# Kernel tuning notes

Measured on AMD Instinct MI355X. Metric: run time of the kernel, lower is better.

Reference implementation:

```python
import jax, jax.numpy as jnp
import numpy as np

N = 262144      # total nodes
G = 256         # graphs
P = 1024        # nodes per graph (k=None sort pool keeps all)
E = 4194304     # edges
F_IN = 128
H = 32
C = 10          # out capsules / classes
OUT_LEN = 16
IN_LEN = 96     # 3 * 32 concat
NUM_ITERS = 3


def setup_inputs() -> dict:
    key = jax.random.key(0)
    ks = jax.random.split(key, 12)
    x = jax.random.normal(ks[0], (N, F_IN), jnp.float32)
    # edges within each graph of size P
    src = jax.random.randint(ks[1], (E,), 0, N)
    off = jax.random.randint(ks[2], (E,), 0, P)
    dst = (src // P) * P + off
    edge_index = jnp.stack([src, dst]).astype(jnp.int64)
    batch = jnp.repeat(jnp.arange(G), P).astype(jnp.int64)
    W1 = jax.random.normal(ks[3], (F_IN, H), jnp.float32) / np.sqrt(F_IN)
    b1 = jnp.zeros((H,), jnp.float32)
    W2 = jax.random.normal(ks[4], (H, H), jnp.float32) / np.sqrt(H)
    b2 = jnp.zeros((H,), jnp.float32)
    W3 = jax.random.normal(ks[5], (H, H), jnp.float32) / np.sqrt(H)
    b3 = jnp.zeros((H,), jnp.float32)
    caps_W = jax.random.normal(ks[6], (C, OUT_LEN, IN_LEN), jnp.float32) * 0.05
    return {"x": x, "edge_index": edge_index, "batch": batch,
            "W1": W1, "b1": b1, "W2": W2, "b2": b2, "W3": W3, "b3": b3,
            "caps_W": caps_W}


def _position_encoding(length, dim):
    pos = jnp.arange(length, dtype=jnp.float32)[:, None]
    i = jnp.arange(dim // 2, dtype=jnp.float32)[None, :]
    ang = pos / jnp.power(10000.0, 2.0 * i / dim)
    return jnp.stack([jnp.sin(ang), jnp.cos(ang)], axis=-1).reshape(length, dim)


def _squash(v, eps=1e-12):
    n2 = jnp.sum(v * v, axis=-1, keepdims=True)
    return (n2 / (1.0 + n2)) * v / jnp.sqrt(n2 + eps)


def reference(x, edge_index, batch, W1, b1, W2, b2, W3, b3, caps_W):
    src, dst = edge_index[0], edge_index[1]
    # remove_self_loops, then GCNConv re-adds self loops with weight 1
    mask = (src != dst).astype(x.dtype)
    deg = jax.ops.segment_sum(mask, dst, num_segments=N) + 1.0
    dis = jax.lax.rsqrt(deg)                         # deg^{-1/2}
    enorm = dis[src] * dis[dst] * mask               # [E]

    def gcn(h, W, b):
        h = h @ W                                    # [N,H]
        agg = jax.ops.segment_sum(h[src] * enorm[:, None], dst, num_segments=N)
        agg = agg + h * (dis * dis)[:, None]         # self-loop term deg^{-1}
        return jnp.tanh(agg + b)

    x1 = gcn(x, W1, b1)
    x2 = gcn(x1, W2, b2)
    x3 = gcn(x2, W3, b3)
    h = jnp.concatenate([x1, x2, x3], axis=-1)       # [N, 96]

    # global_sort_pool (k=None): per-graph sort by last channel, descending
    hg = h.reshape(G, P, IN_LEN)
    order = jnp.argsort(-hg[:, :, -1], axis=1)
    hs = jnp.take_along_axis(hg, order[:, :, None], axis=1)  # [G,P,96]
    hs = hs + _position_encoding(P, IN_LEN)[None]

    # CapsuleLinear, shared weight: priors [G, C, P, OUT_LEN]
    priors = jnp.einsum('oji,gki->gokj', caps_W, hs)

    # k-means routing
    v = jnp.mean(priors, axis=2, keepdims=True)      # [G,C,1,OUT_LEN]
    for _ in range(NUM_ITERS):
        vn = v / (jnp.linalg.norm(v, axis=-1, keepdims=True) + 1e-12)
        logits = jnp.sum(priors * vn, axis=-1, keepdims=True)  # [G,C,P,1]
        prob = jax.nn.softmax(logits, axis=2)
        v = jnp.sum(prob * priors, axis=2, keepdims=True)
    out = _squash(v)[:, :, 0, :]                     # [G, C, OUT_LEN]
    return jnp.linalg.norm(out, axis=-1)             # [G, C]
```

## Files before the change

### kernel.cpp

```cpp
#include <hip/hip_runtime.h>
#include <hip/hip_fp16.h>
#include <cstdint>
#include <cstddef>

#define N_NODES   262144
#define NG        256
#define PP        1024
#define NE        4194304
#define FIN       128
#define HH        32
#define NC        10
#define OL        16
#define IL        96
#define NITER     3
#define ECHUNK    4096
#define NCHUNK    (NE/ECHUNK)
#define ECAP      18432
#define HSTR      36

typedef _Float16 half8 __attribute__((ext_vector_type(8)));
typedef float f32x4 __attribute__((ext_vector_type(4)));

__global__ void k_hist(const int* __restrict__ ei, unsigned* __restrict__ histT) {
  __shared__ unsigned lh[NG];
  int t = threadIdx.x, b = blockIdx.x;
  lh[t] = 0;
  __syncthreads();
  int base = b * ECHUNK;
  for (int q = t; q < ECHUNK; q += 256) {
    int e = base + q;
    int s = ei[e], d = ei[NE + e];
    if (s != d) atomicAdd(&lh[s >> 10], 1u);
  }
  __syncthreads();
  histT[t * NCHUNK + b] = lh[t];
}

__global__ void k_scanA(const unsigned* __restrict__ histT, unsigned* __restrict__ cbaseT,
                        unsigned* __restrict__ gtot) {
  __shared__ unsigned wtot[4];
  int t = threadIdx.x, g = blockIdx.x;
  int lane = t & 63, wv = t >> 6;
  uint4 hv = *(const uint4*)(histT + (size_t)g * NCHUNK + t * 4);
  unsigned s0 = hv.x, s1 = s0 + hv.y, s2 = s1 + hv.z, s3 = s2 + hv.w;
  unsigned tsum = s3, sc = tsum;
  for (int d = 1; d < 64; d <<= 1) {
    unsigned v = __shfl_up(sc, d, 64);
    if (lane >= d) sc += v;
  }
  if (lane == 63) wtot[wv] = sc;
  __syncthreads();
  unsigned woff = 0;
  for (int w = 0; w < wv; ++w) woff += wtot[w];
  unsigned base = woff + sc - tsum;
  cbaseT[(size_t)(t * 4 + 0) * NG + g] = base;
  cbaseT[(size_t)(t * 4 + 1) * NG + g] = base + s0;
  cbaseT[(size_t)(t * 4 + 2) * NG + g] = base + s1;
  cbaseT[(size_t)(t * 4 + 3) * NG + g] = base + s2;
  if (t == 255) gtot[g] = woff + sc;
}

__global__ void k_scanB(const unsigned* __restrict__ gtot, unsigned* __restrict__ gbase) {
  __shared__ unsigned wtot[4];
  int t = threadIdx.x;
  int lane = t & 63, wv = t >> 6;
  unsigned x = gtot[t], sc = x;
  for (int d = 1; d < 64; d <<= 1) {
    unsigned v = __shfl_up(sc, d, 64);
    if (lane >= d) sc += v;
  }
  if (lane == 63) wtot[wv] = sc;
  __syncthreads();
  unsigned woff = 0;
  for (int w = 0; w < wv; ++w) woff += wtot[w];
  gbase[t] = woff + sc - x;
  if (t == 255) gbase[256] = woff + sc;
}

__global__ void k_scatter(const int* __restrict__ ei, const unsigned* __restrict__ cbaseT,
                          const unsigned* __restrict__ gbase, unsigned* __restrict__ epack) {
  __shared__ unsigned lcur[NG];
  int t = threadIdx.x, b = blockIdx.x;
  lcur[t] = gbase[t] + cbaseT[(size_t)b * NG + t];
  __syncthreads();
  int base = b * ECHUNK;
  for (int q = t; q < ECHUNK; q += 256) {
    int e = base + q;
    int s = ei[e], d = ei[NE + e];
    if (s != d) {
      int g = s >> 10;
      unsigned pos = atomicAdd(&lcur[g], 1u);
      epack[pos] = (unsigned)(s & 1023) | ((unsigned)(d & 1023) << 10);
    }
  }
}

__global__ __launch_bounds__(256) void k_dstsort(const unsigned* __restrict__ epack,
                          const unsigned* __restrict__ gbase,
                          unsigned short* __restrict__ esrc16,
                          unsigned* __restrict__ dstptr) {
  __shared__ unsigned shist[PP];
  __shared__ unsigned wsum[256];
  __shared__ unsigned cur[PP];
  int t = threadIdx.x, g = blockIdx.x;
  unsigned e0 = gbase[g], e1 = gbase[g + 1];
  for (int i = t; i < PP; i += 256) shist[i] = 0;
  __syncthreads();
  for (unsigned e = e0 + t; e < e1; e += 256)
    atomicAdd(&shist[(epack[e] >> 10) & 1023], 1u);
  __syncthreads();
  unsigned h0 = shist[4 * t], h1 = shist[4 * t + 1], h2 = shist[4 * t + 2], h3 = shist[4 * t + 3];
  unsigned tsum = h0 + h1 + h2 + h3;
  wsum[t] = tsum;
  __syncthreads();
  for (int off = 1; off < 256; off <<= 1) {
    unsigned v = (t >= off) ? wsum[t - off] : 0u;
    __syncthreads();
    wsum[t] += v;
    __syncthreads();
  }
  unsigned excl = wsum[t] - tsum;
  unsigned c0 = excl, c1 = c0 + h0, c2 = c1 + h1, c3 = c2 + h2;
  cur[4 * t] = c0; cur[4 * t + 1] = c1; cur[4 * t + 2] = c2; cur[4 * t + 3] = c3;
  unsigned* dp = dstptr + (size_t)g * (PP + 1);
  dp[4 * t] = c0; dp[4 * t + 1] = c1; dp[4 * t + 2] = c2; dp[4 * t + 3] = c3;
  if (t == 0) dp[PP] = e1 - e0;
  __syncthreads();
  unsigned short* eg = esrc16 + (size_t)g * ECAP;
  for (unsigned e = e0 + t; e < e1; e += 256) {
    unsigned pk = epack[e];
    unsigned so = pk & 1023, dofs = (pk >> 10) & 1023;
    unsigned pos = atomicAdd(&cur[dofs], 1u);
    if (pos < ECAP) eg[pos] = (unsigned short)so;
  }
}

__global__ void k_dis(const unsigned* __restrict__ dstptr, float* __restrict__ dis) {
  int n = blockIdx.x * 256 + threadIdx.x;
  int g = n >> 10, k = n & 1023;
  const unsigned* dp = dstptr + (size_t)g * (PP + 1) + k;
  float deg = (float)(dp[1] - dp[0]);
  dis[n] = 1.0f / sqrtf(deg + 1.0f);
}

__global__ __launch_bounds__(256) void k_gemm(const float* __restrict__ xin, int ldx, int K,
                                              const float* __restrict__ W,
                                              float* __restrict__ out) {
  __shared__ float Wt[32 * (FIN + 4)];
  int t = threadIdx.x, b = blockIdx.x;
  int stride = K + 4;
  for (int idx = t; idx < K * 32; idx += 256) {
    int k = idx >> 5, c = idx & 31;
    Wt[c * stride + k] = W[idx];
  }
  __syncthreads();
  int cg = t & 3, ng = t >> 2;
  int row0 = b * 128 + ng * 2;
  float acc[2][8];
#pragma unroll
  for (int r = 0; r < 2; ++r)
#pragma unroll
    for (int j = 0; j < 8; ++j) acc[r][j] = 0.f;
  const float* x0 = xin + (size_t)row0 * ldx;
  const float* x1 = xin + (size_t)(row0 + 1) * ldx;
  for (int k4 = 0; k4 < (K >> 2); ++k4) {
    float4 xv0 = *(const float4*)(x0 + k4 * 4);
    float4 xv1 = *(const float4*)(x1 + k4 * 4);
    float4 wvv[8];
#pragma unroll
    for (int j = 0; j < 8; ++j)
      wvv[j] = *(const float4*)&Wt[(cg + 4 * j) * stride + k4 * 4];
#pragma unroll
    for (int j = 0; j < 8; ++j) {
      acc[0][j] += xv0.x * wvv[j].x + xv0.y * wvv[j].y + xv0.z * wvv[j].z + xv0.w * wvv[j].w;
      acc[1][j] += xv1.x * wvv[j].x + xv1.y * wvv[j].y + xv1.z * wvv[j].z + xv1.w * wvv[j].w;
    }
  }
#pragma unroll
  for (int r = 0; r < 2; ++r)
#pragma unroll
    for (int j = 0; j < 8; ++j)
      out[(size_t)(row0 + r) * HH + cg + 4 * j] = acc[r][j];
}

__global__ __launch_bounds__(512) void k_aggf(const float* __restrict__ hlin,
                                              const float* __restrict__ dis,
                                              const unsigned short* __restrict__ esrc16,
                                              const unsigned* __restrict__ dstptr,
                                              const float* __restrict__ bias,
                                              int coloff,
                                              float* __restrict__ h,
                                              const float* __restrict__ Wn,
                                              float* __restrict__ hlin_next) {
  __shared__ float hsl[PP * HSTR];
  int t = threadIdx.x, g = blockIdx.x;
  const float4* hg = (const float4*)(hlin + (size_t)g * PP * HH);
  const float* dg = dis + (size_t)g * PP;
  for (int idx = t; idx < PP * 8; idx += 512) {
    float4 v = hg[idx];
    float d = dg[idx >> 3];
    float4 s;
    s.x = v.x * d; s.y = v.y * d; s.z = v.z * d; s.w = v.w * d;
    *(float4*)&hsl[(idx >> 3) * HSTR + (idx & 7) * 4] = s;
  }
  const unsigned* dp = dstptr + (size_t)g * (PP + 1);
  const unsigned short* eg = esrc16 + (size_t)g * ECAP;
  float4 bl[8];
#pragma unroll
  for (int j = 0; j < 8; ++j) bl[j] = ((const float4*)bias)[j];
  __syncthreads();
#pragma unroll 1
  for (int p = 0; p < 2; ++p) {
    int k = t + p * 512;
    float dk = dg[k];
    unsigned e0 = dp[k], e1 = dp[k + 1];
    float4 acc[8];
    const float* sp = &hsl[k * HSTR];
#pragma unroll
    for (int j = 0; j < 8; ++j) acc[j] = *(const float4*)(sp + 4 * j);
    unsigned e = e0;
    for (; e + 1 < e1; e += 2) {
      int s0 = eg[e], s1 = eg[e + 1];
      const float* q0 = &hsl[s0 * HSTR];
      const float* q1 = &hsl[s1 * HSTR];
#pragma unroll
      for (int j = 0; j < 8; ++j) {
        float4 a = *(const float4*)(q0 + 4 * j);
        float4 b2 = *(const float4*)(q1 + 4 * j);
        acc[j].x += a.x + b2.x; acc[j].y += a.y + b2.y;
        acc[j].z += a.z + b2.z; acc[j].w += a.w + b2.w;
      }
    }
    if (e < e1) {
      int s0 = eg[e];
      const float* q0 = &hsl[s0 * HSTR];
#pragma unroll
      for (int j = 0; j < 8; ++j) {
        float4 a = *(const float4*)(q0 + 4 * j);
        acc[j].x += a.x; acc[j].y += a.y; acc[j].z += a.z; acc[j].w += a.w;
      }
    }
    float xn[32];
#pragma unroll
    for (int j = 0; j < 8; ++j) {
      xn[4 * j + 0] = tanhf(dk * acc[j].x + bl[j].x);
      xn[4 * j + 1] = tanhf(dk * acc[j].y + bl[j].y);
      xn[4 * j + 2] = tanhf(dk * acc[j].z + bl[j].z);
      xn[4 * j + 3] = tanhf(dk * acc[j].w + bl[j].w);
    }
    float* hr = h + (size_t)(g * PP + k) * IL + coloff;
#pragma unroll
    for (int j = 0; j < 8; ++j) {
      float4 s;
      s.x = xn[4 * j]; s.y = xn[4 * j + 1]; s.z = xn[4 * j + 2]; s.w = xn[4 * j + 3];
      *(float4*)(hr + 4 * j) = s;
    }
    if (Wn) {
      float4 o4[8];
#pragma unroll
      for (int j = 0; j < 8; ++j) { o4[j].x = 0.f; o4[j].y = 0.f; o4[j].z = 0.f; o4[j].w = 0.f; }
#pragma unroll
      for (int c = 0; c < 32; ++c) {
        float xc = xn[c];
        const float4* wr = (const float4*)(Wn + c * 32);
#pragma unroll
        for (int j = 0; j < 8; ++j) {
          float4 w = wr[j];
          o4[j].x += xc * w.x; o4[j].y += xc * w.y;
          o4[j].z += xc * w.z; o4[j].w += xc * w.w;
        }
      }
      float* orow = hlin_next + (size_t)(g * PP + k) * HH;
#pragma unroll
      for (int j = 0; j < 8; ++j) *(float4*)(orow + 4 * j) = o4[j];
    }
  }
}

__global__ void k_sort(const float* __restrict__ h, unsigned short* __restrict__ rank16) {
  __shared__ float key[PP];
  __shared__ unsigned sidx[PP];
  int t = threadIdx.x, g = blockIdx.x;
  for (int i = t; i < PP; i += 256) {
    key[i] = h[(size_t)(g * PP + i) * IL + (IL - 1)];
    sidx[i] = i;
  }
  __syncthreads();
  for (int sz = 2; sz <= PP; sz <<= 1) {
    for (int st = sz >> 1; st > 0; st >>= 1) {
      for (int q = t; q < PP / 2; q += 256) {
        int i = 2 * q - (q & (st - 1));
        int j = i + st;
        float ki = key[i], kj = key[j];
        unsigned ii = sidx[i], ij = sidx[j];
        bool less_ji = (kj > ki) || (kj == ki && ij < ii);
        bool asc = ((i & sz) == 0);
        if (less_ji == asc) { key[i] = kj; key[j] = ki; sidx[i] = ij; sidx[j] = ii; }
      }
      __syncthreads();
    }
  }
  for (int i = t; i < PP; i += 256) rank16[g * PP + sidx[i]] = (unsigned short)i;
}

__global__ void k_pe(float* __restrict__ pe) {
  int id = blockIdx.x * 256 + threadIdx.x;
  if (id >= PP * 48) return;
  int pos = id / 48, i = id % 48;
  float denom = powf(10000.0f, (2.0f * i) / 96.0f);
  float ang = (float)pos / denom;
  pe[pos * IL + 2 * i] = sinf(ang);
  pe[pos * IL + 2 * i + 1] = cosf(ang);
}

__global__ void k_wpe(const float* __restrict__ pe, const float* __restrict__ capsW,
                      __half* __restrict__ wpe) {
  int id = blockIdx.x * 256 + threadIdx.x;
  if (id >= NC * PP * OL) return;
  int j = id & 15;
  int pos = (id >> 4) & 1023;
  int c = id >> 14;
  const float* wr = capsW + (size_t)(c * OL + j) * IL;
  const float* pr = pe + (size_t)pos * IL;
  float a = 0;
#pragma unroll 8
  for (int i = 0; i < IL; ++i) a += wr[i] * pr[i];
  wpe[(((size_t)c << 10) + pos) * 16 + j] = __float2half(a);
}

__global__ __launch_bounds__(256) void k_pgemm(const float* __restrict__ h,
                                               const float* __restrict__ capsW,
                                               __half* __restrict__ Pc) {
  int t = threadIdx.x, b = blockIdx.x;
  int g = b >> 2;
  int wv = t >> 6, lane = t & 63;
  int quad = lane >> 4, l16 = lane & 15;
  half8 afr[4][3];
#pragma unroll
  for (int rt = 0; rt < 4; ++rt) {
    int row = b * 256 + wv * 64 + rt * 16 + l16;
    const float* hr = h + (size_t)row * IL + quad * 8;
#pragma unroll
    for (int kb = 0; kb < 3; ++kb) {
      float4 x = *(const float4*)(hr + kb * 32);
      float4 y = *(const float4*)(hr + kb * 32 + 4);
      half8 a;
      a[0] = (_Float16)x.x; a[1] = (_Float16)x.y; a[2] = (_Float16)x.z; a[3] = (_Float16)x.w;
      a[4] = (_Float16)y.x; a[5] = (_Float16)y.y; a[6] = (_Float16)y.z; a[7] = (_Float16)y.w;
      afr[rt][kb] = a;
    }
  }
  int krow_base = (b & 3) * 256 + wv * 64;
  for (int ct = 0; ct < NC; ++ct) {
    half8 bfr[3];
    const float* wr = capsW + (size_t)(ct * 16 + l16) * IL + quad * 8;
#pragma unroll
    for (int kb = 0; kb < 3; ++kb) {
      float4 x = *(const float4*)(wr + kb * 32);
      float4 y = *(const float4*)(wr + kb * 32 + 4);
      half8 bb;
      bb[0] = (_Float16)x.x; bb[1] = (_Float16)x.y; bb[2] = (_Float16)x.z; bb[3] = (_Float16)x.w;
      bb[4] = (_Float16)y.x; bb[5] = (_Float16)y.y; bb[6] = (_Float16)y.z; bb[7] = (_Float16)y.w;
      bfr[kb] = bb;
    }
#pragma unroll
    for (int rt = 0; rt < 4; ++rt) {
      f32x4 acc = {0.f, 0.f, 0.f, 0.f};
      acc = __builtin_amdgcn_mfma_f32_16x16x32_f16(afr[rt][0], bfr[0], acc, 0, 0, 0);
      acc = __builtin_amdgcn_mfma_f32_16x16x32_f16(afr[rt][1], bfr[1], acc, 0, 0, 0);
      acc = __builtin_amdgcn_mfma_f32_16x16x32_f16(afr[rt][2], bfr[2], acc, 0, 0, 0);
      int krow = krow_base + rt * 16;
      __half* po = Pc + ((((size_t)g * NC + ct) << 10) + krow) * 16 + l16;
#pragma unroll
      for (int r = 0; r < 4; ++r)
        po[(quad * 4 + r) * 16] = __float2half(acc[r]);
    }
  }
}

__global__ __launch_bounds__(256) void k_route2(const __half* __restrict__ Pc,
                                                const __half* __restrict__ wpe,
                                                const unsigned short* __restrict__ rank16,
                                                float* __restrict__ out) {
  __shared__ float v_l[16];
  __shared__ float wred[4][17];
  int t = threadIdx.x;
  int gc = blockIdx.x;
  int g = gc / NC, c = gc - g * NC;
  int lane = t & 63, wv = t >> 6;
  const __half* pg = Pc + ((size_t)gc << 10) * 16;
  const unsigned short* rk = rank16 + (size_t)g * PP;
  const __half* wc = wpe + ((size_t)c << 10) * 16;
  float pr[4][16];
  float vsum[16];
#pragma unroll
  for (int i = 0; i < 16; ++i) vsum[i] = 0.f;
#pragma unroll
  for (int r = 0; r < 4; ++r) {
    int k = t + r * 256;
    uint4 a0 = *(const uint4*)(pg + (size_t)k * 16);
    uint4 a1 = *(const uint4*)(pg + (size_t)k * 16 + 8);
    int rkk = rk[k];
    uint4 b0 = *(const uint4*)(wc + (size_t)rkk * 16);
    uint4 b1 = *(const uint4*)(wc + (size_t)rkk * 16 + 8);
    const __half2* pa0 = (const __half2*)&a0; const __half2* pa1 = (const __half2*)&a1;
    const __half2* pb0 = (const __half2*)&b0; const __half2* pb1 = (const __half2*)&b1;
#pragma unroll
    for (int j = 0; j < 4; ++j) {
      float2 fa = __half22float2(pa0[j]); float2 fb = __half22float2(pb0[j]);
      pr[r][2 * j] = fa.x + fb.x; pr[r][2 * j + 1] = fa.y + fb.y;
      float2 fa1 = __half22float2(pa1[j]); float2 fb1 = __half22float2(pb1[j]);
      pr[r][8 + 2 * j] = fa1.x + fb1.x; pr[r][8 + 2 * j + 1] = fa1.y + fb1.y;
    }
#pragma unroll
    for (int i = 0; i < 16; ++i) vsum[i] += pr[r][i];
  }
#pragma unroll
  for (int d = 1; d < 64; d <<= 1)
#pragma unroll
    for (int i = 0; i < 16; ++i) vsum[i] += __shfl_xor(vsum[i], d, 64);
  if (lane == 0) {
#pragma unroll
    for (int i = 0; i < 16; ++i) wred[wv][i] = vsum[i];
  }
  __syncthreads();
  if (t < 16) v_l[t] = wred[0][t] + wred[1][t] + wred[2][t] + wred[3][t];
  __syncthreads();
  for (int it = 0; it < NITER; ++it) {
    float vn[16]; float n2 = 0;
#pragma unroll
    for (int i = 0; i < 16; ++i) { float x = v_l[i]; vn[i] = x; n2 += x * x; }
    float inv = 1.0f / (sqrtf(n2) + 1e-12f);
#pragma unroll
    for (int i = 0; i < 16; ++i) vn[i] *= inv;
    float lg[4];
#pragma unroll
    for (int r = 0; r < 4; ++r) {
      float a = 0;
#pragma unroll
      for (int i = 0; i < 16; ++i) a += pr[r][i] * vn[i];
      lg[r] = a;
    }
    float mx = fmaxf(fmaxf(lg[0], lg[1]), fmaxf(lg[2], lg[3]));
#pragma unroll
    for (int d = 1; d < 64; d <<= 1) mx = fmaxf(mx, __shfl_xor(mx, d, 64));
    __syncthreads();
    if (lane == 0) wred[wv][16] = mx;
    __syncthreads();
    float gmax = fmaxf(fmaxf(wred[0][16], wred[1][16]), fmaxf(wred[2][16], wred[3][16]));
    float es = 0; float eacc[16];
#pragma unroll
    for (int i = 0; i < 16; ++i) eacc[i] = 0.f;
#pragma unroll
    for (int r = 0; r < 4; ++r) {
      float e = __expf(lg[r] - gmax);
      es += e;
#pragma unroll
      for (int i = 0; i < 16; ++i) eacc[i] += e * pr[r][i];
    }
#pragma unroll
    for (int d = 1; d < 64; d <<= 1) {
      es += __shfl_xor(es, d, 64);
#pragma unroll
      for (int i = 0; i < 16; ++i) eacc[i] += __shfl_xor(eacc[i], d, 64);
    }
    __syncthreads();
    if (lane == 0) {
#pragma unroll
      for (int i = 0; i < 16; ++i) wred[wv][i] = eacc[i];
      wred[wv][16] = es;
    }
    __syncthreads();
    if (t < 16) {
      float s = wred[0][t] + wred[1][t] + wred[2][t] + wred[3][t];
      float S = wred[0][16] + wred[1][16] + wred[2][16] + wred[3][16];
      v_l[t] = s / S;
    }
    __syncthreads();
  }
  if (t == 0) {
    float n2 = 0;
#pragma unroll
    for (int i = 0; i < 16; ++i) { float x = v_l[i]; n2 += x * x; }
    out[gc] = (n2 / (1.0f + n2)) * sqrtf(n2) / sqrtf(n2 + 1e-12f);
  }
}

extern "C" void kernel_launch(void* const* d_in, const int* in_sizes, int n_in,
                              void* d_out, int out_size, void* d_ws, size_t ws_size,
                              hipStream_t stream) {
  const float* x     = (const float*)d_in[0];
  const int*   ei    = (const int*)d_in[1];
  const float* W1    = (const float*)d_in[3];
  const float* b1    = (const float*)d_in[4];
  const float* W2    = (const float*)d_in[5];
  const float* b2    = (const float*)d_in[6];
  const float* W3    = (const float*)d_in[7];
  const float* b3    = (const float*)d_in[8];
  const float* capsW = (const float*)d_in[9];
  float* out = (float*)d_out;

  char* wp = (char*)d_ws;
  auto alloc = [&](size_t bytes) { char* p = wp; wp += (bytes + 255) & ~(size_t)255; return p; };
  float*    dis    = (float*)alloc((size_t)N_NODES * 4);
  float*    h      = (float*)alloc((size_t)N_NODES * IL * 4);
  char*     ureg   = wp;
  float*    hlinA  = (float*)alloc((size_t)N_NODES * HH * 4);
  float*    hlinB  = (float*)alloc((size_t)N_NODES * HH * 4);
  unsigned short* esrc16 = (unsigned short*)alloc((size_t)NG * ECAP * 2);
  unsigned* histT  = (unsigned*)alloc((size_t)NCHUNK * NG * 4);
  unsigned* cbaseT = (unsigned*)alloc((size_t)NCHUNK * NG * 4);
  unsigned* epack  = (unsigned*)hlinA;
  const size_t PC_BYTES = (size_t)NG * NC * PP * 16 * 2;
  if ((size_t)(wp - ureg) < PC_BYTES) wp = ureg + ((PC_BYTES + 255) & ~(size_t)255);
  __half*   Pc     = (__half*)ureg;
  unsigned* gtot   = (unsigned*)alloc((size_t)NG * 4);
  unsigned* gbase  = (unsigned*)alloc((size_t)(NG + 1) * 4);
  unsigned* dstptr = (unsigned*)alloc((size_t)NG * (PP + 1) * 4);
  unsigned short* rank16 = (unsigned short*)alloc((size_t)NG * PP * 2);
  float*    pe     = (float*)alloc((size_t)PP * IL * 4);
  __half*   wpe    = (__half*)alloc((size_t)NC * PP * OL * 2);

  k_hist<<<NCHUNK, 256, 0, stream>>>(ei, histT);
  k_scanA<<<NG, 256, 0, stream>>>(histT, cbaseT, gtot);
  k_scanB<<<1, 256, 0, stream>>>(gtot, gbase);
  k_scatter<<<NCHUNK, 256, 0, stream>>>(ei, cbaseT, gbase, epack);
  k_dstsort<<<NG, 256, 0, stream>>>(epack, gbase, esrc16, dstptr);
  k_dis<<<N_NODES / 256, 256, 0, stream>>>(dstptr, dis);
  k_pe<<<(PP * 48) / 256, 256, 0, stream>>>(pe);
  k_wpe<<<(NC * PP * OL) / 256, 256, 0, stream>>>(pe, capsW, wpe);

  k_gemm<<<N_NODES / 128, 256, 0, stream>>>(x, FIN, FIN, W1, hlinA);
  k_aggf<<<NG, 512, 0, stream>>>(hlinA, dis, esrc16, dstptr, b1, 0,  h, W2, hlinB);
  k_aggf<<<NG, 512, 0, stream>>>(hlinB, dis, esrc16, dstptr, b2, 32, h, W3, hlinA);
  k_aggf<<<NG, 512, 0, stream>>>(hlinA, dis, esrc16, dstptr, b3, 64, h, nullptr, nullptr);

  k_sort<<<NG, 256, 0, stream>>>(h, rank16);
  k_pgemm<<<N_NODES / 256, 256, 0, stream>>>(h, capsW, Pc);
  k_route2<<<NG * NC, 256, 0, stream>>>(Pc, wpe, rank16, out);
}
```

Measured before the change: 647.4 us.

## Fuse first GEMM and all three GCN layers into one per-graph kernel

Replaces the separate input GEMM and three aggregation launches with a single per-graph kernel. The kernel keeps the scaled linear features in shared memory across layers and stages each weight matrix in a spare column slot of the shared tile. This removes the global round-trips of the intermediate hlin buffers and three launches. In exchange, the first GEMM now runs on only 256 blocks, which may underuse the GPU and raise register pressure. The bitonic sort also moves to 512 threads, so each compare step is handled by a single pass per thread.

```diff
diff --git a/kernel.cpp b/kernel.cpp
--- a/kernel.cpp
+++ b/kernel.cpp
@@ -143,77 +143,26 @@
   dis[n] = 1.0f / sqrtf(deg + 1.0f);
 }
 
-__global__ __launch_bounds__(256) void k_gemm(const float* __restrict__ xin, int ldx, int K,
-                                              const float* __restrict__ W,
-                                              float* __restrict__ out) {
-  __shared__ float Wt[32 * (FIN + 4)];
-  int t = threadIdx.x, b = blockIdx.x;
-  int stride = K + 4;
-  for (int idx = t; idx < K * 32; idx += 256) {
-    int k = idx >> 5, c = idx & 31;
-    Wt[c * stride + k] = W[idx];
-  }
-  __syncthreads();
-  int cg = t & 3, ng = t >> 2;
-  int row0 = b * 128 + ng * 2;
-  float acc[2][8];
-#pragma unroll
-  for (int r = 0; r < 2; ++r)
-#pragma unroll
-    for (int j = 0; j < 8; ++j) acc[r][j] = 0.f;
-  const float* x0 = xin + (size_t)row0 * ldx;
-  const float* x1 = xin + (size_t)(row0 + 1) * ldx;
-  for (int k4 = 0; k4 < (K >> 2); ++k4) {
-    float4 xv0 = *(const float4*)(x0 + k4 * 4);
-    float4 xv1 = *(const float4*)(x1 + k4 * 4);
-    float4 wvv[8];
-#pragma unroll
-    for (int j = 0; j < 8; ++j)
-      wvv[j] = *(const float4*)&Wt[(cg + 4 * j) * stride + k4 * 4];
-#pragma unroll
-    for (int j = 0; j < 8; ++j) {
-      acc[0][j] += xv0.x * wvv[j].x + xv0.y * wvv[j].y + xv0.z * wvv[j].z + xv0.w * wvv[j].w;
-      acc[1][j] += xv1.x * wvv[j].x + xv1.y * wvv[j].y + xv1.z * wvv[j].z + xv1.w * wvv[j].w;
-    }
-  }
-#pragma unroll
-  for (int r = 0; r < 2; ++r)
-#pragma unroll
-    for (int j = 0; j < 8; ++j)
-      out[(size_t)(row0 + r) * HH + cg + 4 * j] = acc[r][j];
-}
-
-__global__ __launch_bounds__(512) void k_aggf(const float* __restrict__ hlin,
-                                              const float* __restrict__ dis,
-                                              const unsigned short* __restrict__ esrc16,
-                                              const unsigned* __restrict__ dstptr,
-                                              const float* __restrict__ bias,
-                                              int coloff,
-                                              float* __restrict__ h,
-                                              const float* __restrict__ Wn,
-                                              float* __restrict__ hlin_next) {
-  __shared__ float hsl[PP * HSTR];
-  int t = threadIdx.x, g = blockIdx.x;
-  const float4* hg = (const float4*)(hlin + (size_t)g * PP * HH);
-  const float* dg = dis + (size_t)g * PP;
-  for (int idx = t; idx < PP * 8; idx += 512) {
-    float4 v = hg[idx];
-    float d = dg[idx >> 3];
-    float4 s;
-    s.x = v.x * d; s.y = v.y * d; s.z = v.z * d; s.w = v.w * d;
-    *(float4*)&hsl[(idx >> 3) * HSTR + (idx & 7) * 4] = s;
-  }
-  const unsigned* dp = dstptr + (size_t)g * (PP + 1);
-  const unsigned short* eg = esrc16 + (size_t)g * ECAP;
+__device__ __forceinline__ void gcn_layer(float* hsl, const float* dg, const unsigned* dp,
+                                          const unsigned short* eg, const float* bias,
+                                          int coloff, const float* Wn, float* hbase, int t) {
   float4 bl[8];
 #pragma unroll
   for (int j = 0; j < 8; ++j) bl[j] = ((const float4*)bias)[j];
-  __syncthreads();
-#pragma unroll 1
-  for (int p = 0; p < 2; ++p) {
-    int k = t + p * 512;
+  if (Wn) {
+#pragma unroll
+    for (int pp = 0; pp < 8; ++pp) {
+      int p = t + pp * 512;
+      hsl[(p >> 2) * HSTR + 32 + (p & 3)] = Wn[p];
+    }
+  }
+  float xn[2][32];
+#pragma unroll
+  for (int pth = 0; pth < 2; ++pth) {
+    int k = t + pth * 512;
     float dk = dg[k];
     unsigned e0 = dp[k], e1 = dp[k + 1];
+    if (e1 > (unsigned)ECAP) e1 = ECAP;
     float4 acc[8];
     const float* sp = &hsl[k * HSTR];
 #pragma unroll
@@ -240,67 +189,145 @@
         acc[j].x += a.x; acc[j].y += a.y; acc[j].z += a.z; acc[j].w += a.w;
       }
     }
-    float xn[32];
 #pragma unroll
     for (int j = 0; j < 8; ++j) {
-      xn[4 * j + 0] = tanhf(dk * acc[j].x + bl[j].x);
-      xn[4 * j + 1] = tanhf(dk * acc[j].y + bl[j].y);
-      xn[4 * j + 2] = tanhf(dk * acc[j].z + bl[j].z);
-      xn[4 * j + 3] = tanhf(dk * acc[j].w + bl[j].w);
-    }
-    float* hr = h + (size_t)(g * PP + k) * IL + coloff;
+      xn[pth][4 * j + 0] = tanhf(dk * acc[j].x + bl[j].x);
+      xn[pth][4 * j + 1] = tanhf(dk * acc[j].y + bl[j].y);
+      xn[pth][4 * j + 2] = tanhf(dk * acc[j].z + bl[j].z);
+      xn[pth][4 * j + 3] = tanhf(dk * acc[j].w + bl[j].w);
+    }
+    float* hr = hbase + (size_t)k * IL + coloff;
 #pragma unroll
     for (int j = 0; j < 8; ++j) {
       float4 s;
-      s.x = xn[4 * j]; s.y = xn[4 * j + 1]; s.z = xn[4 * j + 2]; s.w = xn[4 * j + 3];
+      s.x = xn[pth][4 * j]; s.y = xn[pth][4 * j + 1];
+      s.z = xn[pth][4 * j + 2]; s.w = xn[pth][4 * j + 3];
       *(float4*)(hr + 4 * j) = s;
     }
-    if (Wn) {
+  }
+  __syncthreads();
+  if (Wn) {
+#pragma unroll
+    for (int pth = 0; pth < 2; ++pth) {
+      int k = t + pth * 512;
+      float dk = dg[k];
       float4 o4[8];
 #pragma unroll
       for (int j = 0; j < 8; ++j) { o4[j].x = 0.f; o4[j].y = 0.f; o4[j].z = 0.f; o4[j].w = 0.f; }
 #pragma unroll
       for (int c = 0; c < 32; ++c) {
-        float xc = xn[c];
-        const float4* wr = (const float4*)(Wn + c * 32);
-#pragma unroll
-        for (int j = 0; j < 8; ++j) {
-          float4 w = wr[j];
-          o4[j].x += xc * w.x; o4[j].y += xc * w.y;
-          o4[j].z += xc * w.z; o4[j].w += xc * w.w;
+        float xc = xn[pth][c];
+#pragma unroll
+        for (int j4 = 0; j4 < 8; ++j4) {
+          float4 w = *(const float4*)&hsl[(c * 8 + j4) * HSTR + 32];
+          o4[j4].x += xc * w.x; o4[j4].y += xc * w.y;
+          o4[j4].z += xc * w.z; o4[j4].w += xc * w.w;
         }
       }
-      float* orow = hlin_next + (size_t)(g * PP + k) * HH;
-#pragma unroll
-      for (int j = 0; j < 8; ++j) *(float4*)(orow + 4 * j) = o4[j];
-    }
-  }
-}
-
-__global__ void k_sort(const float* __restrict__ h, unsigned short* __restrict__ rank16) {
+      float* op = &hsl[k * HSTR];
+#pragma unroll
+      for (int j4 = 0; j4 < 8; ++j4) {
+        float4 s;
+        s.x = o4[j4].x * dk; s.y = o4[j4].y * dk;
+        s.z = o4[j4].z * dk; s.w = o4[j4].w * dk;
+        *(float4*)(op + 4 * j4) = s;
+      }
+    }
+    __syncthreads();
+  }
+}
+
+__global__ __launch_bounds__(512) void k_gcn(const float* __restrict__ x,
+                                             const float* __restrict__ dis,
+                                             const unsigned short* __restrict__ esrc16,
+                                             const unsigned* __restrict__ dstptr,
+                                             const float* __restrict__ W1, const float* __restrict__ b1,
+                                             const float* __restrict__ W2, const float* __restrict__ b2,
+                                             const float* __restrict__ W3, const float* __restrict__ b3,
+                                             float* __restrict__ h) {
+  __shared__ float hsl[PP * HSTR];
+  int t = threadIdx.x, g = blockIdx.x;
+  const float* dg = dis + (size_t)g * PP;
+  const unsigned* dp = dstptr + (size_t)g * (PP + 1);
+  const unsigned short* eg = esrc16 + (size_t)g * ECAP;
+  float* hbase = h + (size_t)g * PP * IL;
+
+#pragma unroll
+  for (int pp = 0; pp < 8; ++pp) {
+    int p = t + pp * 512;
+    hsl[(p >> 2) * HSTR + 32 + (p & 3)] = W1[p];
+  }
+  __syncthreads();
+
+  {
+    int cg = t & 3, ng = t >> 2;
+    int row0 = ng * 8;
+    const float* xr = x + ((size_t)g * PP + row0) * FIN;
+    float acc[8][8];
+#pragma unroll
+    for (int r = 0; r < 8; ++r)
+#pragma unroll
+      for (int j = 0; j < 8; ++j) acc[r][j] = 0.f;
+    for (int k4 = 0; k4 < FIN / 4; ++k4) {
+      float4 xv[8];
+#pragma unroll
+      for (int r = 0; r < 8; ++r)
+        xv[r] = *(const float4*)(xr + (size_t)r * FIN + k4 * 4);
+#pragma unroll
+      for (int kk = 0; kk < 4; ++kk) {
+        int k = k4 * 4 + kk;
+        float4 wa = *(const float4*)&hsl[(k * 8 + cg * 2) * HSTR + 32];
+        float4 wb = *(const float4*)&hsl[(k * 8 + cg * 2 + 1) * HSTR + 32];
+#pragma unroll
+        for (int r = 0; r < 8; ++r) {
+          float xk = kk == 0 ? xv[r].x : kk == 1 ? xv[r].y : kk == 2 ? xv[r].z : xv[r].w;
+          acc[r][0] += xk * wa.x; acc[r][1] += xk * wa.y;
+          acc[r][2] += xk * wa.z; acc[r][3] += xk * wa.w;
+          acc[r][4] += xk * wb.x; acc[r][5] += xk * wb.y;
+          acc[r][6] += xk * wb.z; acc[r][7] += xk * wb.w;
+        }
+      }
+    }
+#pragma unroll
+    for (int r = 0; r < 8; ++r) {
+      float d = dg[row0 + r];
+      float4 s0, s1;
+      s0.x = acc[r][0] * d; s0.y = acc[r][1] * d; s0.z = acc[r][2] * d; s0.w = acc[r][3] * d;
+      s1.x = acc[r][4] * d; s1.y = acc[r][5] * d; s1.z = acc[r][6] * d; s1.w = acc[r][7] * d;
+      *(float4*)&hsl[(row0 + r) * HSTR + cg * 8] = s0;
+      *(float4*)&hsl[(row0 + r) * HSTR + cg * 8 + 4] = s1;
+    }
+  }
+  __syncthreads();
+
+  gcn_layer(hsl, dg, dp, eg, b1, 0,  W2, hbase, t);
+  gcn_layer(hsl, dg, dp, eg, b2, 32, W3, hbase, t);
+  gcn_layer(hsl, dg, dp, eg, b3, 64, nullptr, hbase, t);
+}
+
+__global__ __launch_bounds__(512) void k_sort(const float* __restrict__ h,
+                                              unsigned short* __restrict__ rank16) {
   __shared__ float key[PP];
   __shared__ unsigned sidx[PP];
   int t = threadIdx.x, g = blockIdx.x;
-  for (int i = t; i < PP; i += 256) {
+  for (int i = t; i < PP; i += 512) {
     key[i] = h[(size_t)(g * PP + i) * IL + (IL - 1)];
     sidx[i] = i;
   }
   __syncthreads();
   for (int sz = 2; sz <= PP; sz <<= 1) {
     for (int st = sz >> 1; st > 0; st >>= 1) {
-      for (int q = t; q < PP / 2; q += 256) {
-        int i = 2 * q - (q & (st - 1));
-        int j = i + st;
-        float ki = key[i], kj = key[j];
-        unsigned ii = sidx[i], ij = sidx[j];
-        bool less_ji = (kj > ki) || (kj == ki && ij < ii);
-        bool asc = ((i & sz) == 0);
-        if (less_ji == asc) { key[i] = kj; key[j] = ki; sidx[i] = ij; sidx[j] = ii; }
-      }
+      int i = 2 * t - (t & (st - 1));
+      int j = i + st;
+      float ki = key[i], kj = key[j];
+      unsigned ii = sidx[i], ij = sidx[j];
+      bool less_ji = (kj > ki) || (kj == ki && ij < ii);
+      bool asc = ((i & sz) == 0);
+      if (less_ji == asc) { key[i] = kj; key[j] = ki; sidx[i] = ij; sidx[j] = ii; }
       __syncthreads();
     }
   }
-  for (int i = t; i < PP; i += 256) rank16[g * PP + sidx[i]] = (unsigned short)i;
+  for (int i = t; i < PP; i += 512) rank16[g * PP + sidx[i]] = (unsigned short)i;
 }
 
 __global__ void k_pe(float* __restrict__ pe) {
@@ -505,12 +532,10 @@
   float*    dis    = (float*)alloc((size_t)N_NODES * 4);
   float*    h      = (float*)alloc((size_t)N_NODES * IL * 4);
   char*     ureg   = wp;
-  float*    hlinA  = (float*)alloc((size_t)N_NODES * HH * 4);
-  float*    hlinB  = (float*)alloc((size_t)N_NODES * HH * 4);
+  unsigned* epack  = (unsigned*)alloc((size_t)NE * 4);
   unsigned short* esrc16 = (unsigned short*)alloc((size_t)NG * ECAP * 2);
   unsigned* histT  = (unsigned*)alloc((size_t)NCHUNK * NG * 4);
   unsigned* cbaseT = (unsigned*)alloc((size_t)NCHUNK * NG * 4);
-  unsigned* epack  = (unsigned*)hlinA;
   const size_t PC_BYTES = (size_t)NG * NC * PP * 16 * 2;
   if ((size_t)(wp - ureg) < PC_BYTES) wp = ureg + ((PC_BYTES + 255) & ~(size_t)255);
   __half*   Pc     = (__half*)ureg;
@@ -530,12 +555,9 @@
   k_pe<<<(PP * 48) / 256, 256, 0, stream>>>(pe);
   k_wpe<<<(NC * PP * OL) / 256, 256, 0, stream>>>(pe, capsW, wpe);
 
-  k_gemm<<<N_NODES / 128, 256, 0, stream>>>(x, FIN, FIN, W1, hlinA);
-  k_aggf<<<NG, 512, 0, stream>>>(hlinA, dis, esrc16, dstptr, b1, 0,  h, W2, hlinB);
-  k_aggf<<<NG, 512, 0, stream>>>(hlinB, dis, esrc16, dstptr, b2, 32, h, W3, hlinA);
-  k_aggf<<<NG, 512, 0, stream>>>(hlinA, dis, esrc16, dstptr, b3, 64, h, nullptr, nullptr);
-
-  k_sort<<<NG, 256, 0, stream>>>(h, rank16);
+  k_gcn<<<NG, 512, 0, stream>>>(x, dis, esrc16, dstptr, W1, b1, W2, b2, W3, b3, h);
+
+  k_sort<<<NG, 512, 0, stream>>>(h, rank16);
   k_pgemm<<<N_NODES / 256, 256, 0, stream>>>(h, capsW, Pc);
   k_route2<<<NG * NC, 256, 0, stream>>>(Pc, wpe, rank16, out);
 }
```

Measured after the change: 628.6 us. 2.9% less time.
